# Performance work log

Measured on AMD Instinct MI355X. Metric: run time of the kernel, lower is better.

The kernel has to match this reference:

```python
import jax, jax.numpy as jnp
import numpy as np

B, S, D = 2, 4096, 256
H, DH, DM = 8, 32, 1024
ROPE_BASE = 10000.0
LN_EPS = 1e-5


def _layer_norm(x, g, b):
    mu = jnp.mean(x, axis=-1, keepdims=True)
    var = jnp.mean(jnp.square(x - mu), axis=-1, keepdims=True)
    return (x - mu) * jax.lax.rsqrt(var + LN_EPS) * g + b


def _rope(x):
    # x: [b, s, h, d_head]; lucidrains interleaved-pair RoPE
    s, d = x.shape[1], x.shape[-1]
    inv_freq = 1.0 / (ROPE_BASE ** (jnp.arange(0, d, 2, dtype=jnp.float32) / d))  # [d/2]
    freqs = jnp.arange(s, dtype=jnp.float32)[:, None] * inv_freq[None, :]          # [s, d/2]
    freqs = jnp.repeat(freqs, 2, axis=-1)                                          # [s, d]
    cos = jnp.cos(freqs)[None, :, None, :]
    sin = jnp.sin(freqs)[None, :, None, :]
    x1, x2 = x[..., 0::2], x[..., 1::2]
    rot = jnp.stack((-x2, x1), axis=-1).reshape(x.shape)
    return x * cos + rot * sin


def setup_inputs() -> dict:
    key = jax.random.key(0)
    ks = jax.random.split(key, 8)
    sw = 1.0 / np.sqrt(D)
    return {
        "x": jax.random.normal(ks[0], (B, S, D), jnp.float32),
        "Wq": jax.random.normal(ks[1], (D, D), jnp.float32) * sw,
        "Wk": jax.random.normal(ks[2], (D, D), jnp.float32) * sw,
        "Wv": jax.random.normal(ks[3], (D, D), jnp.float32) * sw,
        "Wo": jax.random.normal(ks[4], (D, D), jnp.float32) * sw,
        "ln1_g": jnp.ones((D,), jnp.float32),
        "ln1_b": jnp.zeros((D,), jnp.float32),
        "ln2_g": jnp.ones((D,), jnp.float32),
        "ln2_b": jnp.zeros((D,), jnp.float32),
        "W2": jax.random.normal(ks[5], (DM, D), jnp.float32) * sw,
        "b2": jnp.zeros((DM,), jnp.float32),
        "W3": jax.random.normal(ks[6], (D, DM), jnp.float32) * (1.0 / np.sqrt(DM)),
        "b3": jnp.zeros((D,), jnp.float32),
    }


def reference(x, Wq, Wk, Wv, Wo, ln1_g, ln1_b, ln2_g, ln2_b, W2, b2, W3, b3):
    b, s, d = x.shape
    h, dh = H, DH
    xn = _layer_norm(x, ln1_g, ln1_b)
    q = (xn @ Wq.T).reshape(b, s, h, dh)
    k = (xn @ Wk.T).reshape(b, s, h, dh)
    v = (xn @ Wv.T).reshape(b, s, h, dh)
    q = _rope(q)
    k = _rope(k)
    # scores: [b, h, q, k] (full matrix, matching original implementation)
    scores = jnp.einsum('bqhd,bkhd->bhqk', q, k) / np.sqrt(dh)
    attn = jax.nn.softmax(scores, axis=-1)
    out = jnp.einsum('bhqk,bkhd->bqhd', attn, v).reshape(b, s, d)
    out = out @ Wo.T
    mlp_in = out + x
    y = _layer_norm(mlp_in, ln2_g, ln2_b)
    y = jax.nn.gelu(y @ W2.T + b2, approximate=False)
    y = y @ W3.T + b3
    return y + mlp_in
```

## Files before the change

### kernel.cpp

```cpp
#include <hip/hip_runtime.h>
#include <math.h>

#define D 256
#define S 4096
#define H 8
#define DH 32
#define DM 1024
#define NTOK 8192

typedef __attribute__((ext_vector_type(8))) short short8;
typedef __attribute__((ext_vector_type(4))) float f32x4;

#define QSCALE (0.17677669529663687f * 1.4426950408889634f)

__device__ inline unsigned short f2bf(float f) {
    union { float f; unsigned u; } v; v.f = f;
    unsigned r = v.u + 0x7fffu + ((v.u >> 16) & 1u);
    return (unsigned short)(r >> 16);
}
__device__ inline void gload16(const void* g, void* l) {
    __builtin_amdgcn_global_load_lds((const __attribute__((address_space(1))) void*)g,
                                     (__attribute__((address_space(3))) void*)l, 16, 0, 0);
}

__global__ void conv_all(const float* __restrict__ Wq, const float* __restrict__ Wk,
                         const float* __restrict__ Wv, const float* __restrict__ Wo,
                         const float* __restrict__ W2, const float* __restrict__ W3,
                         unsigned short* __restrict__ wqkv, unsigned short* __restrict__ wo_b,
                         unsigned short* __restrict__ w2_b, unsigned short* __restrict__ w3_b,
                         float* __restrict__ ct, float* __restrict__ st) {
    int i = blockIdx.x * 256 + threadIdx.x;
    if (i < 196608) {
        const float* s = (i < 65536) ? Wq : ((i < 131072) ? Wk : Wv);
        wqkv[i] = f2bf(s[i & 65535]);
    } else if (i < 262144) {
        wo_b[i - 196608] = f2bf(Wo[i - 196608]);
    } else if (i < 524288) {
        w2_b[i - 262144] = f2bf(W2[i - 262144]);
    } else if (i < 786432) {
        w3_b[i - 524288] = f2bf(W3[i - 524288]);
    } else {
        int j = i - 786432;
        int spos = j >> 4, pi = j & 15;
        float inv_freq = powf(10000.0f, -(float)(2 * pi) / 32.0f);
        float fr = (float)spos * inv_freq;
        ct[j] = cosf(fr);
        st[j] = sinf(fr);
    }
}

__global__ void ln_kernel(const float* __restrict__ x, const float* __restrict__ g,
                          const float* __restrict__ b, unsigned short* __restrict__ out) {
    __shared__ float red[8];
    int row = blockIdx.x;
    int tid = threadIdx.x;
    float v = x[(size_t)row * D + tid];
    float s = v, s2 = v * v;
    #pragma unroll
    for (int off = 32; off > 0; off >>= 1) {
        s  += __shfl_xor(s, off, 64);
        s2 += __shfl_xor(s2, off, 64);
    }
    int wave = tid >> 6;
    if ((tid & 63) == 0) { red[wave] = s; red[wave + 4] = s2; }
    __syncthreads();
    float sum   = red[0] + red[1] + red[2] + red[3];
    float sumsq = red[4] + red[5] + red[6] + red[7];
    float mu  = sum * (1.0f / D);
    float var = sumsq * (1.0f / D) - mu * mu;
    float rs  = rsqrtf(var + 1e-5f);
    out[(size_t)row * D + tid] = f2bf((v - mu) * rs * g[tid] + b[tid]);
}

__global__ __launch_bounds__(256) void gemm64(const unsigned short* __restrict__ A,
        const unsigned short* __restrict__ Bw, void* __restrict__ outp,
        unsigned short* __restrict__ vt,
        const float* __restrict__ bias, const float* __restrict__ res,
        const float* __restrict__ ct, const float* __restrict__ st,
        int N, int K, int mode) {
    __shared__ unsigned short As[2][64 * 32];
    __shared__ unsigned short Bs[2][64 * 32];
    int tid = threadIdx.x;
    int w = tid >> 6, l = tid & 63;
    int lm = l & 15, lg = l >> 4;
    int wm = (w >> 1) * 32, wn = (w & 1) * 32;
    int bm = blockIdx.x * 64, bn = blockIdx.y * 64;
    const unsigned short* Ag = A + (size_t)(bm + w * 16 + (l >> 2)) * K + ((l & 3) ^ ((l >> 3) & 3)) * 8;
    const unsigned short* Bg = Bw + (size_t)(bn + w * 16 + (l >> 2)) * K + ((l & 3) ^ ((l >> 3) & 3)) * 8;
    const int kswz = (lm >> 1) & 3;
    f32x4 acc[2][2] = {};

    gload16(Ag, &As[0][w * 512]);
    gload16(Bg, &Bs[0][w * 512]);
    #pragma unroll 2
    for (int k0 = 0; k0 < K; k0 += 32) {
        int cur = (k0 >> 5) & 1;
        __syncthreads();
        if (k0 + 32 < K) {
            gload16(Ag + k0 + 32, &As[1 - cur][w * 512]);
            gload16(Bg + k0 + 32, &Bs[1 - cur][w * 512]);
        }
        short8 af[2], bf[2];
        #pragma unroll
        for (int i = 0; i < 2; ++i) af[i] = *(const short8*)&As[cur][(wm + i * 16 + lm) * 32 + (lg ^ kswz) * 8];
        #pragma unroll
        for (int i = 0; i < 2; ++i) bf[i] = *(const short8*)&Bs[cur][(wn + i * 16 + lm) * 32 + (lg ^ kswz) * 8];
        #pragma unroll
        for (int mi = 0; mi < 2; ++mi)
            #pragma unroll
            for (int ni = 0; ni < 2; ++ni)
                acc[mi][ni] = __builtin_amdgcn_mfma_f32_16x16x32_bf16(af[mi], bf[ni], acc[mi][ni], 0, 0, 0);
    }

    if (mode == 0) {
        if (bn >= 512) {
            #pragma unroll
            for (int mi = 0; mi < 2; ++mi) {
                #pragma unroll
                for (int ni = 0; ni < 2; ++ni) {
                    int ng = bn + wn + ni * 16 + lm - 512;
                    int hh = ng >> 5, dh = ng & 31;
                    int mg0 = bm + wm + mi * 16 + lg * 4;
                    int bb = mg0 >> 12, ss = mg0 & 4095;
                    ushort4 pv;
                    pv.x = f2bf(acc[mi][ni][0]); pv.y = f2bf(acc[mi][ni][1]);
                    pv.z = f2bf(acc[mi][ni][2]); pv.w = f2bf(acc[mi][ni][3]);
                    *(ushort4*)(vt + ((size_t)((bb * 8 + hh) * 32 + dh)) * S + ss) = pv;
                }
            }
        } else {
            #pragma unroll
            for (int mi = 0; mi < 2; ++mi) {
                #pragma unroll
                for (int ni = 0; ni < 2; ++ni) {
                    int ng = bn + wn + ni * 16 + lm;
                    int pi = (ng & 31) >> 1;
                    float sgn = (ng & 1) ? 1.f : -1.f;
                    float qs  = (ng < 256) ? QSCALE : 1.f;
                    #pragma unroll
                    for (int r2 = 0; r2 < 4; ++r2) {
                        int mg = bm + wm + mi * 16 + lg * 4 + r2;
                        int spos = mg & (S - 1);
                        float vv = acc[mi][ni][r2];
                        float pv = __shfl_xor(vv, 1, 64);
                        float cs = ct[spos * 16 + pi];
                        float sn = st[spos * 16 + pi];
                        float ov = (vv * cs + sgn * pv * sn) * qs;
                        ((unsigned short*)outp)[(size_t)mg * N + ng] = f2bf(ov);
                    }
                }
            }
        }
        return;
    }
    #pragma unroll
    for (int mi = 0; mi < 2; ++mi) {
        #pragma unroll
        for (int ni = 0; ni < 2; ++ni) {
            int ng = bn + wn + ni * 16 + lm;
            #pragma unroll
            for (int r2 = 0; r2 < 4; ++r2) {
                int mg = bm + wm + mi * 16 + lg * 4 + r2;
                float v = acc[mi][ni][r2];
                size_t idx = (size_t)mg * N + ng;
                if (mode == 1) {
                    ((float*)outp)[idx] = v + res[idx];
                } else if (mode == 2) {
                    float t = v + bias[ng];
                    ((unsigned short*)outp)[idx] = f2bf(0.5f * t * (1.0f + erff(t * 0.70710678118654752f)));
                } else {
                    ((float*)outp)[idx] = v + bias[ng] + res[idx];
                }
            }
        }
    }
}

__global__ __launch_bounds__(512) void attn_kernel(const unsigned short* __restrict__ Cq,
        const unsigned short* __restrict__ vt, unsigned short* __restrict__ out) {
    __shared__ unsigned short Ks[2][2][64][32];
    __shared__ unsigned short Vs[2][2][32][64];
    __shared__ unsigned short Ones[16][64];
    int tid = threadIdx.x;
    int w = tid >> 6, l = tid & 63;
    int grp = w >> 2, ws = w & 3;
    int lm = l & 15, lg = l >> 4;
    int qt = blockIdx.x >> 4;
    int bh = blockIdx.x & 15;
    int bb = bh >> 3, h = bh & 7;
    int q0 = qt * 64 + ws * 16;

    if (tid < 256) {
        unsigned short val = (tid < 16) ? (unsigned short)0x3F80 : (unsigned short)0;
        *(ushort4*)(&Ones[0][0] + tid * 4) = make_ushort4(val, val, val, val);
    }

    const short8 qf = *(const short8*)(Cq + ((size_t)(bb * S + q0 + lm)) * 768 + h * DH + lg * 8);
    int p = ws * 16 + (l >> 2);
    int krow = ((p >> 5) << 5) + (((p >> 2) & 3) << 3) + (((p >> 4) & 1) << 2) + (p & 3);
    const unsigned short* kg = Cq + ((size_t)(bb * S)) * 768 + 256 + h * 32
                               + (size_t)krow * 768 + ((l & 3) ^ ((l >> 3) & 3)) * 8;
    const unsigned short* vg = vt + ((size_t)(bh * 32 + ws * 8 + (l >> 3))) * S + ((l & 7) ^ (l >> 3)) * 8;
    const int kswz = (lm >> 1) & 3;
    const int vswz = lm & 7;

    f32x4 o0 = {0.f, 0.f, 0.f, 0.f}, o1 = {0.f, 0.f, 0.f, 0.f}, o2 = {0.f, 0.f, 0.f, 0.f};
    const f32x4 z = {0.f, 0.f, 0.f, 0.f};

    gload16(kg + (size_t)grp * 64 * 768, &Ks[grp][0][ws * 16][0]);
    gload16(vg + (size_t)grp * 64,       &Vs[grp][0][ws * 8][0]);

    #pragma unroll 2
    for (int it = 0; it < S / 128; ++it) {
        int cur = it & 1;
        __syncthreads();
        if (it + 1 < S / 128) {
            size_t t = (size_t)(2 * (it + 1) + grp);
            gload16(kg + t * 64 * 768, &Ks[grp][1 - cur][ws * 16][0]);
            gload16(vg + t * 64,       &Vs[grp][1 - cur][ws * 8][0]);
        }
        #pragma unroll
        for (int half = 0; half < 2; ++half) {
            short8 kf0 = *(const short8*)&Ks[grp][cur][half * 32 + lm][(lg ^ kswz) * 8];
            short8 kf1 = *(const short8*)&Ks[grp][cur][half * 32 + 16 + lm][(lg ^ kswz) * 8];
            f32x4 s0 = __builtin_amdgcn_mfma_f32_16x16x32_bf16(kf0, qf, z, 0, 0, 0);
            f32x4 s1 = __builtin_amdgcn_mfma_f32_16x16x32_bf16(kf1, qf, z, 0, 0, 0);
            unsigned u0[4], u1[4];
            #pragma unroll
            for (int i = 0; i < 4; ++i) {
                union { float f; unsigned u; } c0, c1;
                c0.f = __builtin_amdgcn_exp2f(s0[i]);
                c1.f = __builtin_amdgcn_exp2f(s1[i]);
                u0[i] = c0.u;
                u1[i] = c1.u;
            }
            union { unsigned u[4]; short8 s; } pk;
            pk.u[0] = __builtin_amdgcn_perm(u0[1], u0[0], 0x07060302u);
            pk.u[1] = __builtin_amdgcn_perm(u0[3], u0[2], 0x07060302u);
            pk.u[2] = __builtin_amdgcn_perm(u1[1], u1[0], 0x07060302u);
            pk.u[3] = __builtin_amdgcn_perm(u1[3], u1[2], 0x07060302u);
            short8 pf = pk.s;
            int vc = ((half * 4 + lg) ^ vswz) * 8;
            short8 va0 = *(const short8*)&Vs[grp][cur][lm][vc];
            short8 va1 = *(const short8*)&Vs[grp][cur][16 + lm][vc];
            short8 va2 = *(const short8*)&Ones[lm][vc];
            o0 = __builtin_amdgcn_mfma_f32_16x16x32_bf16(va0, pf, o0, 0, 0, 0);
            o1 = __builtin_amdgcn_mfma_f32_16x16x32_bf16(va1, pf, o1, 0, 0, 0);
            o2 = __builtin_amdgcn_mfma_f32_16x16x32_bf16(va2, pf, o2, 0, 0, 0);
        }
    }
    f32x4* Red0 = (f32x4*)&Ks[1][0][0][0];
    f32x4* Red1 = (f32x4*)&Vs[1][0][0][0];
    float* Den  = (float*)&Ones[0][0];
    __syncthreads();
    if (grp) {
        Red0[ws * 64 + l] = o0;
        Red1[ws * 64 + l] = o1;
        Den[ws * 64 + l]  = o2[0];
    }
    __syncthreads();
    if (!grp) {
        f32x4 a0 = Red0[ws * 64 + l];
        f32x4 a1 = Red1[ws * 64 + l];
        float dd = o2[0] + Den[ws * 64 + l];
        #pragma unroll
        for (int i = 0; i < 4; ++i) { o0[i] += a0[i]; o1[i] += a1[i]; }
        float lsum = __shfl(dd, lm, 64);
        float inv = 1.0f / lsum;
        ushort4 r0, r1;
        r0.x = f2bf(o0[0] * inv); r0.y = f2bf(o0[1] * inv);
        r0.z = f2bf(o0[2] * inv); r0.w = f2bf(o0[3] * inv);
        r1.x = f2bf(o1[0] * inv); r1.y = f2bf(o1[1] * inv);
        r1.z = f2bf(o1[2] * inv); r1.w = f2bf(o1[3] * inv);
        unsigned short* ob = out + ((size_t)(bb * S + q0 + lm)) * D + h * DH;
        *(ushort4*)(ob + lg * 4)      = r0;
        *(ushort4*)(ob + 16 + lg * 4) = r1;
    }
}

extern "C" void kernel_launch(void* const* d_in, const int* in_sizes, int n_in,
                              void* d_out, int out_size, void* d_ws, size_t ws_size,
                              hipStream_t stream) {
    const float* x     = (const float*)d_in[0];
    const float* Wq    = (const float*)d_in[1];
    const float* Wk    = (const float*)d_in[2];
    const float* Wv    = (const float*)d_in[3];
    const float* Wo    = (const float*)d_in[4];
    const float* ln1_g = (const float*)d_in[5];
    const float* ln1_b = (const float*)d_in[6];
    const float* ln2_g = (const float*)d_in[7];
    const float* ln2_b = (const float*)d_in[8];
    const float* W2    = (const float*)d_in[9];
    const float* b2    = (const float*)d_in[10];
    const float* W3    = (const float*)d_in[11];
    const float* b3    = (const float*)d_in[12];

    char* w8 = (char*)d_ws;
    unsigned short* wqkv = (unsigned short*)(w8);
    unsigned short* wo_b = (unsigned short*)(w8 + 393216);
    unsigned short* w2_b = (unsigned short*)(w8 + 524288);
    unsigned short* w3_b = (unsigned short*)(w8 + 1048576);
    float*          ct   = (float*)(w8 + 1572864);
    float*          st   = (float*)(w8 + 1835008);
    unsigned short* xn   = (unsigned short*)(w8 + 2097152);
    unsigned short* Cq   = (unsigned short*)(w8 + 6291456);
    unsigned short* hb   = Cq;
    unsigned short* vtb  = (unsigned short*)(w8 + 23068672);
    unsigned short* ab   = (unsigned short*)(w8 + 27262976);
    float*          mlpin= (float*)(w8 + 31457280);
    unsigned short* yn   = xn;

    conv_all<<<3328, 256, 0, stream>>>(Wq, Wk, Wv, Wo, W2, W3, wqkv, wo_b, w2_b, w3_b, ct, st);
    ln_kernel<<<NTOK, 256, 0, stream>>>(x, ln1_g, ln1_b, xn);
    gemm64<<<dim3(128, 12), 256, 0, stream>>>(xn, wqkv, Cq, vtb, nullptr, nullptr, ct, st, 768, 256, 0);
    attn_kernel<<<1024, 512, 0, stream>>>(Cq, vtb, ab);
    gemm64<<<dim3(128, 4), 256, 0, stream>>>(ab, wo_b, mlpin, nullptr, nullptr, x, nullptr, nullptr, 256, 256, 1);
    ln_kernel<<<NTOK, 256, 0, stream>>>(mlpin, ln2_g, ln2_b, yn);
    gemm64<<<dim3(128, 16), 256, 0, stream>>>(yn, w2_b, hb, nullptr, b2, nullptr, nullptr, nullptr, 1024, 256, 2);
    gemm64<<<dim3(128, 4), 256, 0, stream>>>(hb, w3_b, (float*)d_out, nullptr, b3, mlpin, nullptr, nullptr, 256, 1024, 3);
}
```

Before: 204.0 us.

## Double GEMM K-tile to 64 and add 32-row GEMM for narrow outputs

```diff
diff --git a/kernel.cpp b/kernel.cpp
--- a/kernel.cpp
+++ b/kernel.cpp
@@ -72,44 +72,55 @@
     out[(size_t)row * D + tid] = f2bf((v - mu) * rs * g[tid] + b[tid]);
 }
 
-__global__ __launch_bounds__(256) void gemm64(const unsigned short* __restrict__ A,
+__global__ __launch_bounds__(256) void gemm64b(const unsigned short* __restrict__ A,
         const unsigned short* __restrict__ Bw, void* __restrict__ outp,
         unsigned short* __restrict__ vt,
-        const float* __restrict__ bias, const float* __restrict__ res,
+        const float* __restrict__ bias,
         const float* __restrict__ ct, const float* __restrict__ st,
         int N, int K, int mode) {
-    __shared__ unsigned short As[2][64 * 32];
-    __shared__ unsigned short Bs[2][64 * 32];
+    __shared__ unsigned short As[2][64 * 64];
+    __shared__ unsigned short Bs[2][64 * 64];
     int tid = threadIdx.x;
     int w = tid >> 6, l = tid & 63;
     int lm = l & 15, lg = l >> 4;
     int wm = (w >> 1) * 32, wn = (w & 1) * 32;
     int bm = blockIdx.x * 64, bn = blockIdx.y * 64;
-    const unsigned short* Ag = A + (size_t)(bm + w * 16 + (l >> 2)) * K + ((l & 3) ^ ((l >> 3) & 3)) * 8;
-    const unsigned short* Bg = Bw + (size_t)(bn + w * 16 + (l >> 2)) * K + ((l & 3) ^ ((l >> 3) & 3)) * 8;
-    const int kswz = (lm >> 1) & 3;
+    int r1 = tid >> 3, pc = tid & 7;
+    int pcx = (pc ^ (r1 & 7)) * 8;
+    const unsigned short* Ag1 = A + (size_t)(bm + r1) * K + pcx;
+    const unsigned short* Ag2 = A + (size_t)(bm + 32 + r1) * K + pcx;
+    const unsigned short* Bg1 = Bw + (size_t)(bn + r1) * K + pcx;
+    const unsigned short* Bg2 = Bw + (size_t)(bn + 32 + r1) * K + pcx;
+    const int swz = lm & 7;
     f32x4 acc[2][2] = {};
 
-    gload16(Ag, &As[0][w * 512]);
-    gload16(Bg, &Bs[0][w * 512]);
-    #pragma unroll 2
-    for (int k0 = 0; k0 < K; k0 += 32) {
-        int cur = (k0 >> 5) & 1;
+    gload16(Ag1, &As[0][w * 512]);
+    gload16(Ag2, &As[0][2048 + w * 512]);
+    gload16(Bg1, &Bs[0][w * 512]);
+    gload16(Bg2, &Bs[0][2048 + w * 512]);
+    for (int k0 = 0; k0 < K; k0 += 64) {
+        int cur = (k0 >> 6) & 1;
         __syncthreads();
-        if (k0 + 32 < K) {
-            gload16(Ag + k0 + 32, &As[1 - cur][w * 512]);
-            gload16(Bg + k0 + 32, &Bs[1 - cur][w * 512]);
-        }
-        short8 af[2], bf[2];
-        #pragma unroll
-        for (int i = 0; i < 2; ++i) af[i] = *(const short8*)&As[cur][(wm + i * 16 + lm) * 32 + (lg ^ kswz) * 8];
-        #pragma unroll
-        for (int i = 0; i < 2; ++i) bf[i] = *(const short8*)&Bs[cur][(wn + i * 16 + lm) * 32 + (lg ^ kswz) * 8];
-        #pragma unroll
-        for (int mi = 0; mi < 2; ++mi)
-            #pragma unroll
-            for (int ni = 0; ni < 2; ++ni)
-                acc[mi][ni] = __builtin_amdgcn_mfma_f32_16x16x32_bf16(af[mi], bf[ni], acc[mi][ni], 0, 0, 0);
+        if (k0 + 64 < K) {
+            gload16(Ag1 + k0 + 64, &As[1 - cur][w * 512]);
+            gload16(Ag2 + k0 + 64, &As[1 - cur][2048 + w * 512]);
+            gload16(Bg1 + k0 + 64, &Bs[1 - cur][w * 512]);
+            gload16(Bg2 + k0 + 64, &Bs[1 - cur][2048 + w * 512]);
+        }
+        #pragma unroll
+        for (int j = 0; j < 2; ++j) {
+            int ch = ((j * 4 + lg) ^ swz) * 8;
+            short8 af[2], bf[2];
+            #pragma unroll
+            for (int i = 0; i < 2; ++i) af[i] = *(const short8*)&As[cur][(wm + i * 16 + lm) * 64 + ch];
+            #pragma unroll
+            for (int i = 0; i < 2; ++i) bf[i] = *(const short8*)&Bs[cur][(wn + i * 16 + lm) * 64 + ch];
+            #pragma unroll
+            for (int mi = 0; mi < 2; ++mi)
+                #pragma unroll
+                for (int ni = 0; ni < 2; ++ni)
+                    acc[mi][ni] = __builtin_amdgcn_mfma_f32_16x16x32_bf16(af[mi], bf[ni], acc[mi][ni], 0, 0, 0);
+        }
     }
 
     if (mode == 0) {
@@ -161,16 +172,69 @@
             #pragma unroll
             for (int r2 = 0; r2 < 4; ++r2) {
                 int mg = bm + wm + mi * 16 + lg * 4 + r2;
-                float v = acc[mi][ni][r2];
-                size_t idx = (size_t)mg * N + ng;
-                if (mode == 1) {
-                    ((float*)outp)[idx] = v + res[idx];
-                } else if (mode == 2) {
-                    float t = v + bias[ng];
-                    ((unsigned short*)outp)[idx] = f2bf(0.5f * t * (1.0f + erff(t * 0.70710678118654752f)));
-                } else {
-                    ((float*)outp)[idx] = v + bias[ng] + res[idx];
-                }
+                float t = acc[mi][ni][r2] + bias[ng];
+                ((unsigned short*)outp)[(size_t)mg * N + ng] =
+                    f2bf(0.5f * t * (1.0f + erff(t * 0.70710678118654752f)));
+            }
+        }
+    }
+}
+
+__global__ __launch_bounds__(256) void gemm32(const unsigned short* __restrict__ A,
+        const unsigned short* __restrict__ Bw, void* __restrict__ outp,
+        const float* __restrict__ bias, const float* __restrict__ res,
+        int N, int K, int mode) {
+    __shared__ unsigned short As[2][32 * 64];
+    __shared__ unsigned short Bs[2][64 * 64];
+    int tid = threadIdx.x;
+    int w = tid >> 6, l = tid & 63;
+    int lm = l & 15, lg = l >> 4;
+    int rm = (w >> 1) * 16, wn = (w & 1) * 32;
+    int bm = blockIdx.x * 32, bn = blockIdx.y * 64;
+    int r1 = tid >> 3, pc = tid & 7;
+    int pcx = (pc ^ (r1 & 7)) * 8;
+    const unsigned short* Ag1 = A + (size_t)(bm + r1) * K + pcx;
+    const unsigned short* Bg1 = Bw + (size_t)(bn + r1) * K + pcx;
+    const unsigned short* Bg2 = Bw + (size_t)(bn + 32 + r1) * K + pcx;
+    const int swz = lm & 7;
+    f32x4 acc[2] = {};
+
+    gload16(Ag1, &As[0][w * 512]);
+    gload16(Bg1, &Bs[0][w * 512]);
+    gload16(Bg2, &Bs[0][2048 + w * 512]);
+    for (int k0 = 0; k0 < K; k0 += 64) {
+        int cur = (k0 >> 6) & 1;
+        __syncthreads();
+        if (k0 + 64 < K) {
+            gload16(Ag1 + k0 + 64, &As[1 - cur][w * 512]);
+            gload16(Bg1 + k0 + 64, &Bs[1 - cur][w * 512]);
+            gload16(Bg2 + k0 + 64, &Bs[1 - cur][2048 + w * 512]);
+        }
+        #pragma unroll
+        for (int j = 0; j < 2; ++j) {
+            int ch = ((j * 4 + lg) ^ swz) * 8;
+            short8 af = *(const short8*)&As[cur][(rm + lm) * 64 + ch];
+            short8 bf[2];
+            #pragma unroll
+            for (int i = 0; i < 2; ++i) bf[i] = *(const short8*)&Bs[cur][(wn + i * 16 + lm) * 64 + ch];
+            #pragma unroll
+            for (int ni = 0; ni < 2; ++ni)
+                acc[ni] = __builtin_amdgcn_mfma_f32_16x16x32_bf16(af, bf[ni], acc[ni], 0, 0, 0);
+        }
+    }
+
+    #pragma unroll
+    for (int ni = 0; ni < 2; ++ni) {
+        int ng = bn + wn + ni * 16 + lm;
+        #pragma unroll
+        for (int r2 = 0; r2 < 4; ++r2) {
+            int mg = bm + rm + lg * 4 + r2;
+            float v = acc[ni][r2];
+            size_t idx = (size_t)mg * N + ng;
+            if (mode == 1) {
+                ((float*)outp)[idx] = v + res[idx];
+            } else {
+                ((float*)outp)[idx] = v + bias[ng] + res[idx];
             }
         }
     }
@@ -312,10 +376,10 @@
 
     conv_all<<<3328, 256, 0, stream>>>(Wq, Wk, Wv, Wo, W2, W3, wqkv, wo_b, w2_b, w3_b, ct, st);
     ln_kernel<<<NTOK, 256, 0, stream>>>(x, ln1_g, ln1_b, xn);
-    gemm64<<<dim3(128, 12), 256, 0, stream>>>(xn, wqkv, Cq, vtb, nullptr, nullptr, ct, st, 768, 256, 0);
+    gemm64b<<<dim3(128, 12), 256, 0, stream>>>(xn, wqkv, Cq, vtb, nullptr, ct, st, 768, 256, 0);
     attn_kernel<<<1024, 512, 0, stream>>>(Cq, vtb, ab);
-    gemm64<<<dim3(128, 4), 256, 0, stream>>>(ab, wo_b, mlpin, nullptr, nullptr, x, nullptr, nullptr, 256, 256, 1);
+    gemm32<<<dim3(256, 4), 256, 0, stream>>>(ab, wo_b, mlpin, nullptr, x, 256, 256, 1);
     ln_kernel<<<NTOK, 256, 0, stream>>>(mlpin, ln2_g, ln2_b, yn);
-    gemm64<<<dim3(128, 16), 256, 0, stream>>>(yn, w2_b, hb, nullptr, b2, nullptr, nullptr, nullptr, 1024, 256, 2);
-    gemm64<<<dim3(128, 4), 256, 0, stream>>>(hb, w3_b, (float*)d_out, nullptr, b3, mlpin, nullptr, nullptr, 256, 1024, 3);
-}
+    gemm64b<<<dim3(128, 16), 256, 0, stream>>>(yn, w2_b, hb, nullptr, b2, nullptr, nullptr, 1024, 256, 2);
+    gemm32<<<dim3(256, 4), 256, 0, stream>>>(hb, w3_b, (float*)d_out, b3, mlpin, 256, 1024, 3);
+}
```

After: 197.7 us. 1.03x faster.
